# Optimization experiments

Hardware: AMD Instinct MI355X
Metric: run time of the kernel (lower is better)

The kernel has to match this reference:

```python
import jax, jax.numpy as jnp
import numpy as np

B, T, D, H, LAT = 512, 8, 512, 512, 64
NSTEPS = 4  # fixed RK4 steps per observation interval (replaces adaptive dopri5)


def _lin(key, out_dim, in_dim):
    k1, k2 = jax.random.split(key)
    s = 1.0 / np.sqrt(in_dim)
    W = jax.random.uniform(k1, (out_dim, in_dim), minval=-s, maxval=s, dtype=jnp.float32)
    b = jax.random.uniform(k2, (out_dim,), minval=-s, maxval=s, dtype=jnp.float32)
    return W, b


def setup_inputs() -> dict:
    key = jax.random.key(0)
    ks = jax.random.split(key, 8)
    x = jax.random.normal(ks[0], (B, T, D), dtype=jnp.float32)
    # strictly increasing per-sample observation times
    ts = jnp.cumsum(jax.random.uniform(ks[1], (B, T), dtype=jnp.float32) + 0.05, axis=1)
    Wih, bih = _lin(ks[2], 3 * H, D)      # GRU input weights
    Whh, bhh = _lin(ks[3], 3 * H, H)      # GRU hidden weights
    Wout, bout = _lin(ks[4], 2 * LAT, H)  # h2o head: mean/logvar of latent
    W1, b1 = _lin(ks[5], 2 * H, H + 1)    # LatentODEfunc fc1 (state + time)
    W2, b2 = _lin(ks[6], 2 * H, 2 * H)    # fc2
    W3, b3 = _lin(ks[7], H, 2 * H)        # fc3
    return dict(x=x, ts=ts, Wih=Wih, Whh=Whh, bih=bih, bhh=bhh,
                Wout=Wout, bout=bout, W1=W1, b1=b1, W2=W2, b2=b2, W3=W3, b3=b3)


def reference(x, ts, Wih, Whh, bih, bhh, Wout, bout, W1, b1, W2, b2, W3, b3):
    swish = lambda v: v * jax.nn.sigmoid(v)

    def odefunc(t, h):  # t: (B,), h: (B,H) -> dh/dt (B,H)
        z = jnp.concatenate([h, t[:, None]], axis=1)
        z = swish(z @ W1.T + b1)
        z = swish(z @ W2.T + b2)
        return z @ W3.T + b3

    def ode_integrate(h, t0, t1):  # batched RK4 with per-sample dt
        dt = (t1 - t0) / NSTEPS  # (B,)
        def body(carry, _):
            h, t = carry
            d = dt[:, None]
            k1 = odefunc(t, h)
            k2 = odefunc(t + dt / 2, h + d * k1 / 2)
            k3 = odefunc(t + dt / 2, h + d * k2 / 2)
            k4 = odefunc(t + dt, h + d * k3)
            return (h + d / 6 * (k1 + 2 * k2 + 2 * k3 + k4), t + dt), None
        (h, _), _ = jax.lax.scan(body, (h, t0), None, length=NSTEPS)
        return h

    def gru_cell(obs, h):  # torch GRUCell math
        gi = obs @ Wih.T + bih
        gh = h @ Whh.T + bhh
        ir, iz, inn = jnp.split(gi, 3, axis=1)
        hr, hz, hn = jnp.split(gh, 3, axis=1)
        r = jax.nn.sigmoid(ir + hr)
        zg = jax.nn.sigmoid(iz + hz)
        n = jnp.tanh(inn + r * hn)
        return (1.0 - zg) * n + zg * h

    # first interval has zero length -> RK4 with dt=0 leaves h0 unchanged (no ODE at t=0)
    t_prev = jnp.concatenate([ts[:, :1], ts[:, :-1]], axis=1)

    def step(carry, inputs):
        h, c = carry
        obs, t0, t1 = inputs
        h = ode_integrate(h, t0, t1)
        h = gru_cell(obs, h)
        out = h @ Wout.T + bout  # (B, 2*LAT)
        return (h, c), out

    h0 = jnp.zeros((x.shape[0], H), x.dtype)
    c0 = jnp.zeros_like(h0)
    xs = (jnp.swapaxes(x, 0, 1), t_prev.T, ts.T)  # time-major for scan
    (h, c), outs = jax.lax.scan(step, (h0, c0), xs)
    return outs[-1], h, c
```

## Files before the change

kernel.cpp:

```cpp
#include <hip/hip_runtime.h>
#include <hip/hip_bf16.h>
#include <stdint.h>


#define B_ 512
#define T_ 8
#define H_ 512
#define D_ 512

typedef short short8 __attribute__((ext_vector_type(8)));
typedef float f32x4 __attribute__((ext_vector_type(4)));
typedef __hip_bfloat16 bf16;
typedef unsigned long long u64;

__device__ __forceinline__ float sigm(float x){ return 1.f/(1.f+__expf(-x)); }

#define MFMA16(a,b,c) __builtin_amdgcn_mfma_f32_16x16x32_bf16((a),(b),(c),0,0,0)
#define ALD4(p)   __hip_atomic_load((p), __ATOMIC_RELAXED, __HIP_MEMORY_SCOPE_AGENT)
#define AST8(p,v) __hip_atomic_store((u64*)(p),(v),__ATOMIC_RELAXED,__HIP_MEMORY_SCOPE_AGENT)

__device__ __forceinline__ void wait_ge(unsigned* c, unsigned tgt, int* dead){
  if (threadIdx.x == 0){
    if (!*dead){
      int it = 0;
      while (ALD4(c) < tgt){
        __builtin_amdgcn_s_sleep(1);
        if (++it > 50000000){ *dead = 1; break; }
      }
    }
  }
  __syncthreads();
}
__device__ __forceinline__ void publish(unsigned* c){
  __builtin_amdgcn_s_waitcnt(0);
  __syncthreads();
  if (threadIdx.x == 0)
    __hip_atomic_fetch_add(c, 1u, __ATOMIC_RELAXED, __HIP_MEMORY_SCOPE_AGENT);
}

template<int CH, int SH>
__device__ __forceinline__ void stageC16(bf16* lds, int lstr, const bf16* g, int gstr){
  f32x4 tmp[CH];
#pragma unroll
  for (int j = 0; j < CH; ++j){
    int idx = j*256 + threadIdx.x;
    const bf16* p = g + (size_t)(idx >> SH)*gstr + (size_t)(idx & ((1<<SH)-1))*8;
    asm volatile("global_load_dwordx4 %0, %1, off sc0 sc1" : "=v"(tmp[j]) : "v"(p));
  }
  asm volatile("s_waitcnt vmcnt(0)" ::: "memory");
  __builtin_amdgcn_sched_barrier(0);
#pragma unroll
  for (int j = 0; j < CH; ++j){
    int idx = j*256 + threadIdx.x;
    *(f32x4*)&lds[(idx >> SH)*lstr + (idx & ((1<<SH)-1))*8] = tmp[j];
  }
}
template<int CH, int SH>
__device__ __forceinline__ void stageP(bf16* lds, int lstr, const bf16* g, size_t gstr){
#pragma unroll
  for (int j = 0; j < CH; ++j){
    int idx = j*256 + threadIdx.x;
    *(short8*)&lds[(idx >> SH)*lstr + (idx & ((1<<SH)-1))*8] =
        *(const short8*)(g + (size_t)(idx >> SH)*gstr + (size_t)(idx & ((1<<SH)-1))*8);
  }
}

__device__ __forceinline__ u64 pk4(float a0, float a1, float a2, float a3){
  union { bf16 h[4]; u64 q; } u;
  u.h[0] = __float2bfloat16(a0); u.h[1] = __float2bfloat16(a1);
  u.h[2] = __float2bfloat16(a2); u.h[3] = __float2bfloat16(a3);
  return u.q;
}

__global__ __launch_bounds__(256, 1) void persist_k(
    const bf16* __restrict__ W1hb, const bf16* __restrict__ W2b,
    const bf16* __restrict__ Wfb,  const bf16* __restrict__ W3b,
    const bf16* __restrict__ Woutb,const bf16* __restrict__ Wc3,
    const bf16* __restrict__ xbf,
    const float* __restrict__ b1,  const float* __restrict__ b2,
    const float* __restrict__ b3,  const float* __restrict__ bout,
    const float* __restrict__ bcb3,const float* __restrict__ w1t,
    const float* __restrict__ bf3, const float* __restrict__ ts,
    bf16* wbuf, bf16* hbuf, bf16* z1buf, bf16* z2buf, bf16* zbuf,
    unsigned* cnts, float* dout)
{
  extern __shared__ char smem[];
  bf16* slab = (bf16*)smem;
  float* t0s = (float*)(smem + 66048);
  float* dts = (float*)(smem + 66176);
  int* dead  = (int*)(smem + 66304);

  const int tid = threadIdx.x, lane = tid & 63, wv = tid >> 6;
  const int fr = lane & 15, quad = lane >> 4;
  const int nb = blockIdx.x & 15;
  const int mb = blockIdx.x >> 4;
  const int gm0 = mb * 32;
  const int wm = wv & 1;
  const int wn = wv >> 1;

  unsigned* cz1 = cnts + mb*128;
  unsigned* cz2 = cz1 + 32;
  unsigned* ch  = cz1 + 64;
  unsigned* cg  = cz1 + 96;

  if (tid < 32){
    float t0 = ts[(gm0 + tid)*T_];
    t0s[tid] = t0; dts[tid] = 0.f;
  }
  if (tid == 0) *dead = 0;
  __syncthreads();

  const int zc0 = 64*nb + 16*wv + quad*4;
  const int kc0 = 32*nb + 16*wn + quad*4;
  const f32x4 b1v  = *(const f32x4*)&b1[zc0];
  const f32x4 w1tv = *(const f32x4*)&w1t[zc0];
  const f32x4 b2v  = *(const f32x4*)&b2[zc0];
  const f32x4 bf3v = *(const f32x4*)&bf3[zc0];
  const f32x4 b3v  = *(const f32x4*)&b3[kc0];
  f32x4 bcv[4];
#pragma unroll
  for (int g = 0; g < 4; ++g)
    bcv[g] = *(const f32x4*)&bcb3[nb*128 + g*32 + 16*wn + quad*4];
  const f32x4 bov = *(const f32x4*)&bout[16*(nb & 7) + quad*4];

  const bf16* w1p = W1hb  + (size_t)(64*nb + 16*wv + fr)*512  + quad*8;
  const bf16* w2p = W2b   + (size_t)(64*nb + 16*wv + fr)*1024 + quad*8;
  const bf16* wfp = Wfb   + (size_t)(64*nb + 16*wv + fr)*1024 + quad*8;
  const bf16* w3p = W3b   + (size_t)(32*nb + 16*wn + fr)*1024 + quad*8;
  const bf16* wop = Woutb + (size_t)(16*(nb & 7) + fr)*512 + quad*8;
  const bf16* wcp[4];
#pragma unroll
  for (int g = 0; g < 4; ++g)
    wcp[g] = Wc3 + (size_t)(nb*128 + g*32 + 16*wn + fr)*1024 + quad*8;

  short8 w2f[32], wff[32];
#pragma unroll
  for (int k = 0; k < 32; ++k) w2f[k] = *(const short8*)(w2p + k*32);
#pragma unroll
  for (int k = 0; k < 32; ++k) wff[k] = *(const short8*)(wfp + k*32);

  float hw0[4]={0,0,0,0}, hw1[4]={0,0,0,0};
  float pacc0[4]={0,0,0,0}, pacc1[4]={0,0,0,0};
  float zacc0[4]={0,0,0,0}, zacc1[4]={0,0,0,0};
  float hreg[4]={0,0,0,0};
  unsigned tz1 = 16, tz2 = 16, tch = 16, tcg = 16;

  {
    const float t0a = t0s[fr], t0b = t0s[16 + fr];
    float v0[4], v1[4];
#pragma unroll
    for (int j = 0; j < 4; ++j){
      v0[j] = t0a*w1tv[j] + b1v[j];
      v1[j] = t0b*w1tv[j] + b1v[j];
      v0[j] *= sigm(v0[j]); v1[j] *= sigm(v1[j]);
    }
    AST8(z1buf + (size_t)(gm0 + fr)*1024 + zc0,      pk4(v0[0],v0[1],v0[2],v0[3]));
    AST8(z1buf + (size_t)(gm0 + 16 + fr)*1024 + zc0, pk4(v1[0],v1[1],v1[2],v1[3]));
    publish(cz1);
  }

  for (int s = 0; s < T_; ++s){
    for (int sub = 0; sub < 4; ++sub){
      for (int e = 1; e <= 4; ++e){
        wait_ge(cz1, tz1, dead); tz1 += 16;
        stageC16<16,7>(slab, 1032, z1buf + (size_t)gm0*1024, 1024);
        __syncthreads();
        {
          f32x4 a0 = {0,0,0,0}, a1 = {0,0,0,0};
#pragma unroll
          for (int k = 0; k < 32; ++k){
            a0 = MFMA16(w2f[k], *(const short8*)&slab[fr*1032      + k*32 + quad*8], a0);
            a1 = MFMA16(w2f[k], *(const short8*)&slab[(16+fr)*1032 + k*32 + quad*8], a1);
          }
          const float wgt = (e == 2 || e == 3) ? 2.f : 1.f;
          float s0[4], s1[4];
#pragma unroll
          for (int j = 0; j < 4; ++j){
            float v0 = a0[j] + b2v[j], v1 = a1[j] + b2v[j];
            s0[j] = v0*sigm(v0); s1[j] = v1*sigm(v1);
            zacc0[j] += wgt*s0[j]; zacc1[j] += wgt*s1[j];
          }
          if (sub == 3 && e == 4){
            AST8(zbuf + (size_t)(gm0 + fr)*1024 + zc0,      pk4(zacc0[0],zacc0[1],zacc0[2],zacc0[3]));
            AST8(zbuf + (size_t)(gm0 + 16 + fr)*1024 + zc0, pk4(zacc1[0],zacc1[1],zacc1[2],zacc1[3]));
#pragma unroll
            for (int j = 0; j < 4; ++j){ zacc0[j] = 0.f; zacc1[j] = 0.f; }
          } else {
            AST8(z2buf + (size_t)(gm0 + fr)*1024 + zc0,      pk4(s0[0],s0[1],s0[2],s0[3]));
            AST8(z2buf + (size_t)(gm0 + 16 + fr)*1024 + zc0, pk4(s1[0],s1[1],s1[2],s1[3]));
          }
          publish(cz2);
        }
        if (!(sub == 3 && e == 4)){
          wait_ge(cz2, tz2, dead); tz2 += 16;
          stageC16<16,7>(slab, 1032, z2buf + (size_t)gm0*1024, 1024);
          __syncthreads();
          f32x4 p0 = {0,0,0,0}, p1 = {0,0,0,0};
#pragma unroll
          for (int k = 0; k < 32; ++k){
            p0 = MFMA16(wff[k], *(const short8*)&slab[fr*1032      + k*32 + quad*8], p0);
            p1 = MFMA16(wff[k], *(const short8*)&slab[(16+fr)*1032 + k*32 + quad*8], p1);
          }
          const float dta = dts[fr], dtb = dts[16 + fr];
          const float t0a = t0s[fr], t0b = t0s[16 + fr];
          const float ce = (e <= 2) ? (float)sub + 0.5f : (float)sub + 1.f;
          float v0[4], v1[4];
          if (e < 4){
            const float c = (e == 3) ? 1.f : 0.5f;
            const float wgt = (e == 2 || e == 3) ? 2.f : 1.f;
            if (sub < 3){
#pragma unroll
              for (int j = 0; j < 4; ++j){ pacc0[j] += wgt*p0[j]; pacc1[j] += wgt*p1[j]; }
            }
#pragma unroll
            for (int j = 0; j < 4; ++j){
              v0[j] = hw0[j] + c*dta*(p0[j] + bf3v[j]) + (t0a + dta*ce)*w1tv[j] + b1v[j];
              v1[j] = hw1[j] + c*dtb*(p1[j] + bf3v[j]) + (t0b + dtb*ce)*w1tv[j] + b1v[j];
            }
          } else {
#pragma unroll
            for (int j = 0; j < 4; ++j){
              float pa = pacc0[j] + p0[j], pb = pacc1[j] + p1[j];
              hw0[j] += dta*(1.f/6.f)*pa + dta*bf3v[j];
              hw1[j] += dtb*(1.f/6.f)*pb + dtb*bf3v[j];
              pacc0[j] = 0.f; pacc1[j] = 0.f;
              v0[j] = hw0[j] + (t0a + dta*ce)*w1tv[j] + b1v[j];
              v1[j] = hw1[j] + (t0b + dtb*ce)*w1tv[j] + b1v[j];
            }
          }
#pragma unroll
          for (int j = 0; j < 4; ++j){ v0[j] *= sigm(v0[j]); v1[j] *= sigm(v1[j]); }
          AST8(z1buf + (size_t)(gm0 + fr)*1024 + zc0,      pk4(v0[0],v0[1],v0[2],v0[3]));
          AST8(z1buf + (size_t)(gm0 + 16 + fr)*1024 + zc0, pk4(v1[0],v1[1],v1[2],v1[3]));
          publish(cz1);
        }
      }
    }
    wait_ge(cz2, tz2, dead); tz2 += 16;
    stageC16<16,7>(slab, 1032, zbuf + (size_t)gm0*1024, 1024);
    __syncthreads();
    {
      f32x4 ak = {0,0,0,0};
#pragma unroll 8
      for (int k = 0; k < 32; ++k){
        ak = MFMA16(*(const short8*)(w3p + k*32),
                    *(const short8*)&slab[(wm*16 + fr)*1032 + k*32 + quad*8], ak);
      }
      const int r = wm*16 + fr;
      const float dtv = dts[r];
#pragma unroll
      for (int j = 0; j < 4; ++j)
        hreg[j] = hreg[j] + dtv*(1.f/6.f)*ak[j] + 4.f*dtv*b3v[j];
      AST8(hbuf + (size_t)(gm0 + r)*512 + kc0, pk4(hreg[0],hreg[1],hreg[2],hreg[3]));
      publish(ch);
    }
    wait_ge(ch, tch, dead); tch += 16;
    stageC16<8,6>(slab, 1032, hbuf + (size_t)gm0*512, 512);
    stageP<8,6>(slab + 512, 1032, xbf + ((size_t)gm0*T_ + s)*512, (size_t)T_*512);
    __syncthreads();
    {
      f32x4 ag[4] = {{0,0,0,0},{0,0,0,0},{0,0,0,0},{0,0,0,0}};
#pragma unroll 4
      for (int k = 0; k < 32; ++k){
        short8 xv = *(const short8*)&slab[(wm*16 + fr)*1032 + k*32 + quad*8];
#pragma unroll
        for (int g = 0; g < 4; ++g)
          ag[g] = MFMA16(*(const short8*)(wcp[g] + k*32), xv, ag[g]);
      }
      const int r = wm*16 + fr;
#pragma unroll
      for (int j = 0; j < 4; ++j){
        float r_ = sigm(ag[0][j] + bcv[0][j]);
        float z_ = sigm(ag[1][j] + bcv[1][j]);
        float hn = ag[2][j] + bcv[2][j];
        float in = ag[3][j] + bcv[3][j];
        float n_ = tanhf(in + r_*hn);
        hreg[j] = (1.f - z_)*n_ + z_*hreg[j];
      }
      AST8(wbuf + (size_t)(gm0 + r)*512 + kc0, pk4(hreg[0],hreg[1],hreg[2],hreg[3]));
      if (s == T_-1){
        f32x4 hv; hv[0]=hreg[0]; hv[1]=hreg[1]; hv[2]=hreg[2]; hv[3]=hreg[3];
        *(f32x4*)&dout[(size_t)B_*128 + (size_t)(gm0 + r)*512 + kc0] = hv;
        f32x4 z4 = {0,0,0,0};
        *(f32x4*)&dout[(size_t)B_*128 + (size_t)B_*512 + (size_t)(gm0 + r)*512 + kc0] = z4;
      }
      if (tid < 32){
        float t0n = ts[(gm0 + tid)*T_ + s];
        float t1  = (s < T_-1) ? ts[(gm0 + tid)*T_ + s + 1] : t0n;
        t0s[tid] = t0n; dts[tid] = (t1 - t0n)*0.25f;
      }
      publish(cg);
    }
    if (s < T_-1){
      wait_ge(cg, tcg, dead); tcg += 16;
      stageC16<8,6>(slab, 520, wbuf + (size_t)gm0*512, 512);
      __syncthreads();
      f32x4 a0 = {0,0,0,0}, a1 = {0,0,0,0};
#pragma unroll 4
      for (int k = 0; k < 16; ++k){
        short8 wt = *(const short8*)(w1p + k*32);
        a0 = MFMA16(wt, *(const short8*)&slab[fr*520      + k*32 + quad*8], a0);
        a1 = MFMA16(wt, *(const short8*)&slab[(16+fr)*520 + k*32 + quad*8], a1);
      }
      const float t0a = t0s[fr], t0b = t0s[16 + fr];
      float v0[4], v1[4];
#pragma unroll
      for (int j = 0; j < 4; ++j){
        hw0[j] = a0[j]; hw1[j] = a1[j];
        v0[j] = hw0[j] + t0a*w1tv[j] + b1v[j];
        v1[j] = hw1[j] + t0b*w1tv[j] + b1v[j];
        v0[j] *= sigm(v0[j]); v1[j] *= sigm(v1[j]);
      }
      AST8(z1buf + (size_t)(gm0 + fr)*1024 + zc0,      pk4(v0[0],v0[1],v0[2],v0[3]));
      AST8(z1buf + (size_t)(gm0 + 16 + fr)*1024 + zc0, pk4(v1[0],v1[1],v1[2],v1[3]));
      publish(cz1);
    }
  }
  wait_ge(cg, tcg, dead); tcg += 16;
  stageC16<8,6>(slab, 520, wbuf + (size_t)gm0*512, 512);
  __syncthreads();
  if (nb < 8 && wv < 2){
    f32x4 ao = {0,0,0,0};
#pragma unroll 4
    for (int k = 0; k < 16; ++k){
      ao = MFMA16(*(const short8*)(wop + k*32),
                  *(const short8*)&slab[(wv*16 + fr)*520 + k*32 + quad*8], ao);
    }
    f32x4 o;
#pragma unroll
    for (int j = 0; j < 4; ++j) o[j] = ao[j] + bov[j];
    *(f32x4*)&dout[(size_t)(gm0 + wv*16 + fr)*128 + 16*nb + quad*4] = o;
  }
}

__global__ void conv_k(const float* __restrict__ in, bf16* __restrict__ out,
                       int rows, int kin, int kout)
{
  int idx = blockIdx.x*256 + threadIdx.x;
  if (idx >= rows*kout) return;
  int r = idx / kout, k = idx - r*kout;
  out[idx] = __float2bfloat16(k < kin ? in[(size_t)r*kin + k] : 0.f);
}

__global__ void w1t_k(const float* __restrict__ W1, float* __restrict__ w1t)
{
  int i = blockIdx.x*256 + threadIdx.x;
  if (i < 1024) w1t[i] = W1[(size_t)i*513 + 512];
}

__global__ void wf_k(const float* __restrict__ W1, const float* __restrict__ W3,
                     bf16* __restrict__ Wfb)
{
  __shared__ float At[64][64];
  __shared__ float Bt[64][65];
  const int i0 = blockIdx.y*64, j0 = blockIdx.x*64;
  const int tid = threadIdx.x;
  const int ty = tid >> 4, tx = tid & 15;
  float acc[4][4] = {};
  for (int kc = 0; kc < 512; kc += 64){
#pragma unroll
    for (int t = 0; t < 16; ++t){
      int idx = t*256 + tid;
      int r = idx >> 6, k = idx & 63;
      At[r][k] = W1[(size_t)(i0 + r)*513 + kc + k];
      Bt[r][k] = W3[(size_t)(kc + r)*1024 + j0 + k];
    }
    __syncthreads();
#pragma unroll 8
    for (int k = 0; k < 64; ++k){
      float a[4], b[4];
#pragma unroll
      for (int ii = 0; ii < 4; ++ii) a[ii] = At[ty*4 + ii][k];
#pragma unroll
      for (int jj = 0; jj < 4; ++jj) b[jj] = Bt[k][tx*4 + jj];
#pragma unroll
      for (int ii = 0; ii < 4; ++ii)
#pragma unroll
        for (int jj = 0; jj < 4; ++jj) acc[ii][jj] += a[ii]*b[jj];
    }
    __syncthreads();
  }
#pragma unroll
  for (int ii = 0; ii < 4; ++ii)
#pragma unroll
    for (int jj = 0; jj < 4; ++jj)
      Wfb[(size_t)(i0 + ty*4 + ii)*1024 + j0 + tx*4 + jj] = __float2bfloat16(acc[ii][jj]);
}

__global__ void bf3_k(const float* __restrict__ W1, const float* __restrict__ b3,
                      float* __restrict__ bf3)
{
  int i = blockIdx.x*256 + threadIdx.x;
  if (i < 1024){
    float acc = 0.f;
    for (int c = 0; c < 512; ++c) acc += W1[(size_t)i*513 + c]*b3[c];
    bf3[i] = acc;
  }
}

__global__ void wc3_k(const float* __restrict__ Wih, const float* __restrict__ Whh,
                      const float* __restrict__ bih, const float* __restrict__ bhh,
                      bf16* __restrict__ Wc3, float* __restrict__ bcb3)
{
  int idx = blockIdx.x*256 + threadIdx.x;
  if (idx >= 2048*1024) return;
  int R = idx >> 10, k = idx & 1023;
  int n16 = R >> 7, g = (R >> 5) & 3, c = R & 31;
  int hc = n16*32 + c;
  float v;
  if      (g == 0) v = (k < 512) ? Whh[(size_t)hc*512 + k]        : Wih[(size_t)hc*512 + k - 512];
  else if (g == 1) v = (k < 512) ? Whh[(size_t)(512+hc)*512 + k]  : Wih[(size_t)(512+hc)*512 + k - 512];
  else if (g == 2) v = (k < 512) ? Whh[(size_t)(1024+hc)*512 + k] : 0.f;
  else             v = (k < 512) ? 0.f                             : Wih[(size_t)(1024+hc)*512 + k - 512];
  Wc3[idx] = __float2bfloat16(v);
  if (k == 0){
    if      (g == 0) bcb3[R] = bih[hc] + bhh[hc];
    else if (g == 1) bcb3[R] = bih[512 + hc] + bhh[512 + hc];
    else if (g == 2) bcb3[R] = bhh[1024 + hc];
    else             bcb3[R] = bih[1024 + hc];
  }
}

__global__ void init_k(unsigned* __restrict__ cnts)
{
  int idx = blockIdx.x*256 + threadIdx.x;
  if (idx < 16*128) cnts[idx] = 0u;
}

extern "C" void kernel_launch(void* const* d_in, const int* in_sizes, int n_in,
                              void* d_out, int out_size, void* d_ws, size_t ws_size,
                              hipStream_t stream)
{
  const float* x    = (const float*)d_in[0];
  const float* ts   = (const float*)d_in[1];
  const float* Wih  = (const float*)d_in[2];
  const float* Whh  = (const float*)d_in[3];
  const float* bih  = (const float*)d_in[4];
  const float* bhh  = (const float*)d_in[5];
  const float* Wout = (const float*)d_in[6];
  const float* bout = (const float*)d_in[7];
  const float* W1   = (const float*)d_in[8];
  const float* b1   = (const float*)d_in[9];
  const float* W2   = (const float*)d_in[10];
  const float* b2   = (const float*)d_in[11];
  const float* W3   = (const float*)d_in[12];
  const float* b3   = (const float*)d_in[13];

  char* ws = (char*)d_ws;
  size_t off = 0;
  auto alloc = [&](size_t n){ void* p = ws + off; off += (n + 255) & ~(size_t)255; return p; };

  bf16* xbf   = (bf16*)alloc((size_t)B_*T_*D_*2);
  bf16* W1hb  = (bf16*)alloc((size_t)1024*512*2);
  bf16* W2b   = (bf16*)alloc((size_t)1024*1024*2);
  bf16* Wfb   = (bf16*)alloc((size_t)1024*1024*2);
  bf16* W3b   = (bf16*)alloc((size_t)512*1024*2);
  bf16* Woutb = (bf16*)alloc((size_t)128*512*2);
  bf16* Wc3   = (bf16*)alloc((size_t)2048*1024*2);
  float* bcb3 = (float*)alloc((size_t)2048*4);
  float* w1t  = (float*)alloc((size_t)1024*4);
  float* bf3  = (float*)alloc((size_t)1024*4);
  bf16* wbuf  = (bf16*)alloc((size_t)B_*H_*2);
  bf16* hbuf  = (bf16*)alloc((size_t)B_*H_*2);
  bf16* z1buf = (bf16*)alloc((size_t)B_*1024*2);
  bf16* z2buf = (bf16*)alloc((size_t)B_*1024*2);
  bf16* zbuf  = (bf16*)alloc((size_t)B_*1024*2);
  unsigned* cnts = (unsigned*)alloc((size_t)16*128*4);

  auto conv = [&](const float* in, bf16* out, int rows, int kin, int kout){
    int n = rows*kout;
    conv_k<<<(n + 255)/256, 256, 0, stream>>>(in, out, rows, kin, kout);
  };
  conv(x, xbf, B_*T_, D_, D_);
  conv(W1, W1hb, 1024, 513, 512);
  conv(W2, W2b, 1024, 1024, 1024);
  conv(W3, W3b, 512, 1024, 1024);
  conv(Wout, Woutb, 128, 512, 512);
  w1t_k<<<4, 256, 0, stream>>>(W1, w1t);
  wf_k<<<dim3(16,16), 256, 0, stream>>>(W1, W3, Wfb);
  bf3_k<<<4, 256, 0, stream>>>(W1, b3, bf3);
  wc3_k<<<(2048*1024)/256, 256, 0, stream>>>(Wih, Whh, bih, bhh, Wc3, bcb3);
  init_k<<<8, 256, 0, stream>>>(cnts);

  (void)hipFuncSetAttribute((const void*)persist_k,
                            hipFuncAttributeMaxDynamicSharedMemorySize, 66560);
  persist_k<<<256, 256, 66560, stream>>>(
      W1hb, W2b, Wfb, W3b, Woutb, Wc3, xbf,
      b1, b2, b3, bout, bcb3, w1t, bf3, ts,
      wbuf, hbuf, z1buf, z2buf, zbuf, cnts, (float*)d_out);
}
```

Before: 1.822 ms.

## Co-locate row-group blocks on one XCD and use L2-coherent exchange when confirmed

Changes the block-to-tile mapping so the 16 blocks sharing a row group (mb) get block IDs that are congruent mod 8, which under round-robin dispatch should place them on the same XCD. Each block reads its XCC_ID from a hardware register and checks through a global table that all its peers report the same one. If they do, the inter-block exchange buffers are written and read with sc0 only (L2 scope) instead of sc0 sc1 system-coherent accesses, cutting the latency of the per-stage handoffs. This adds a startup handshake, and it depends on the dispatch-placement assumption; when the check fails it falls back to the old coherent path.

Result: faster. 1.565 ms (-14.1%).

```diff
diff --git a/kernel.cpp b/kernel.cpp
--- a/kernel.cpp
+++ b/kernel.cpp
@@ -17,7 +17,6 @@
 
 #define MFMA16(a,b,c) __builtin_amdgcn_mfma_f32_16x16x32_bf16((a),(b),(c),0,0,0)
 #define ALD4(p)   __hip_atomic_load((p), __ATOMIC_RELAXED, __HIP_MEMORY_SCOPE_AGENT)
-#define AST8(p,v) __hip_atomic_store((u64*)(p),(v),__ATOMIC_RELAXED,__HIP_MEMORY_SCOPE_AGENT)
 
 __device__ __forceinline__ void wait_ge(unsigned* c, unsigned tgt, int* dead){
   if (threadIdx.x == 0){
@@ -38,14 +37,21 @@
     __hip_atomic_fetch_add(c, 1u, __ATOMIC_RELAXED, __HIP_MEMORY_SCOPE_AGENT);
 }
 
-template<int CH, int SH>
+template<bool L2C>
+__device__ __forceinline__ void ast8c(void* p, u64 v){
+  if (L2C) asm volatile("global_store_dwordx2 %0, %1, off sc0" :: "v"(p), "v"(v) : "memory");
+  else     __hip_atomic_store((u64*)p, v, __ATOMIC_RELAXED, __HIP_MEMORY_SCOPE_AGENT);
+}
+
+template<int CH, int SH, bool L2C>
 __device__ __forceinline__ void stageC16(bf16* lds, int lstr, const bf16* g, int gstr){
   f32x4 tmp[CH];
 #pragma unroll
   for (int j = 0; j < CH; ++j){
     int idx = j*256 + threadIdx.x;
     const bf16* p = g + (size_t)(idx >> SH)*gstr + (size_t)(idx & ((1<<SH)-1))*8;
-    asm volatile("global_load_dwordx4 %0, %1, off sc0 sc1" : "=v"(tmp[j]) : "v"(p));
+    if (L2C) asm volatile("global_load_dwordx4 %0, %1, off sc0"     : "=v"(tmp[j]) : "v"(p));
+    else     asm volatile("global_load_dwordx4 %0, %1, off sc0 sc1" : "=v"(tmp[j]) : "v"(p));
   }
   asm volatile("s_waitcnt vmcnt(0)" ::: "memory");
   __builtin_amdgcn_sched_barrier(0);
@@ -71,6 +77,8 @@
   u.h[2] = __float2bfloat16(a2); u.h[3] = __float2bfloat16(a3);
   return u.q;
 }
+
+template<bool V> struct BC { static constexpr bool value = V; };
 
 __global__ __launch_bounds__(256, 1) void persist_k(
     const bf16* __restrict__ W1hb, const bf16* __restrict__ W2b,
@@ -82,18 +90,20 @@
     const float* __restrict__ bcb3,const float* __restrict__ w1t,
     const float* __restrict__ bf3, const float* __restrict__ ts,
     bf16* wbuf, bf16* hbuf, bf16* z1buf, bf16* z2buf, bf16* zbuf,
-    unsigned* cnts, float* dout)
+    unsigned* cnts, unsigned* xtab, float* dout)
 {
   extern __shared__ char smem[];
   bf16* slab = (bf16*)smem;
   float* t0s = (float*)(smem + 66048);
   float* dts = (float*)(smem + 66176);
   int* dead  = (int*)(smem + 66304);
+  int* fflag = (int*)(smem + 66308);
 
   const int tid = threadIdx.x, lane = tid & 63, wv = tid >> 6;
   const int fr = lane & 15, quad = lane >> 4;
-  const int nb = blockIdx.x & 15;
-  const int mb = blockIdx.x >> 4;
+  const int bId = blockIdx.x;
+  const int mb = (bId & 7) + 8*(bId >> 7);
+  const int nb = (bId >> 3) & 15;
   const int gm0 = mb * 32;
   const int wm = wv & 1;
   const int wn = wv >> 1;
@@ -103,12 +113,38 @@
   unsigned* ch  = cz1 + 64;
   unsigned* cg  = cz1 + 96;
 
+  unsigned myxcd;
+  asm volatile("s_getreg_b32 %0, hwreg(HW_REG_XCC_ID)" : "=s"(myxcd));
+  myxcd = (myxcd & 0x7fffffffu) | 0x80000000u;
+  if (tid == 0)
+    __hip_atomic_store(&xtab[bId], myxcd, __ATOMIC_RELAXED, __HIP_MEMORY_SCOPE_AGENT);
+
   if (tid < 32){
     float t0 = ts[(gm0 + tid)*T_];
     t0s[tid] = t0; dts[tid] = 0.f;
   }
   if (tid == 0) *dead = 0;
+
+  if (tid == 0){
+    unsigned ref = 0; int ok = 1;
+    for (int j = 0; j < 16; ++j){
+      int bj = (mb & 7) + 8*j + 128*(mb >> 3);
+      unsigned v; int it = 0;
+      do {
+        v = ALD4(&xtab[bj]);
+        if (!v){
+          __builtin_amdgcn_s_sleep(8);
+          if (++it > 200000){ ok = 0; break; }
+        }
+      } while (!v);
+      if (!v){ ok = 0; break; }
+      if (j == 0) ref = v;
+      else if (v != ref){ ok = 0; break; }
+    }
+    *fflag = ok && (ref != 0);
+  }
   __syncthreads();
+  const int fastp = *fflag;
 
   const int zc0 = 64*nb + 16*wv + quad*4;
   const int kc0 = 32*nb + 16*wn + quad*4;
@@ -145,180 +181,186 @@
   float hreg[4]={0,0,0,0};
   unsigned tz1 = 16, tz2 = 16, tch = 16, tcg = 16;
 
-  {
-    const float t0a = t0s[fr], t0b = t0s[16 + fr];
-    float v0[4], v1[4];
-#pragma unroll
-    for (int j = 0; j < 4; ++j){
-      v0[j] = t0a*w1tv[j] + b1v[j];
-      v1[j] = t0b*w1tv[j] + b1v[j];
-      v0[j] *= sigm(v0[j]); v1[j] *= sigm(v1[j]);
-    }
-    AST8(z1buf + (size_t)(gm0 + fr)*1024 + zc0,      pk4(v0[0],v0[1],v0[2],v0[3]));
-    AST8(z1buf + (size_t)(gm0 + 16 + fr)*1024 + zc0, pk4(v1[0],v1[1],v1[2],v1[3]));
-    publish(cz1);
-  }
-
-  for (int s = 0; s < T_; ++s){
-    for (int sub = 0; sub < 4; ++sub){
-      for (int e = 1; e <= 4; ++e){
-        wait_ge(cz1, tz1, dead); tz1 += 16;
-        stageC16<16,7>(slab, 1032, z1buf + (size_t)gm0*1024, 1024);
-        __syncthreads();
-        {
-          f32x4 a0 = {0,0,0,0}, a1 = {0,0,0,0};
-#pragma unroll
-          for (int k = 0; k < 32; ++k){
-            a0 = MFMA16(w2f[k], *(const short8*)&slab[fr*1032      + k*32 + quad*8], a0);
-            a1 = MFMA16(w2f[k], *(const short8*)&slab[(16+fr)*1032 + k*32 + quad*8], a1);
-          }
-          const float wgt = (e == 2 || e == 3) ? 2.f : 1.f;
-          float s0[4], s1[4];
-#pragma unroll
-          for (int j = 0; j < 4; ++j){
-            float v0 = a0[j] + b2v[j], v1 = a1[j] + b2v[j];
-            s0[j] = v0*sigm(v0); s1[j] = v1*sigm(v1);
-            zacc0[j] += wgt*s0[j]; zacc1[j] += wgt*s1[j];
-          }
-          if (sub == 3 && e == 4){
-            AST8(zbuf + (size_t)(gm0 + fr)*1024 + zc0,      pk4(zacc0[0],zacc0[1],zacc0[2],zacc0[3]));
-            AST8(zbuf + (size_t)(gm0 + 16 + fr)*1024 + zc0, pk4(zacc1[0],zacc1[1],zacc1[2],zacc1[3]));
-#pragma unroll
-            for (int j = 0; j < 4; ++j){ zacc0[j] = 0.f; zacc1[j] = 0.f; }
-          } else {
-            AST8(z2buf + (size_t)(gm0 + fr)*1024 + zc0,      pk4(s0[0],s0[1],s0[2],s0[3]));
-            AST8(z2buf + (size_t)(gm0 + 16 + fr)*1024 + zc0, pk4(s1[0],s1[1],s1[2],s1[3]));
-          }
-          publish(cz2);
-        }
-        if (!(sub == 3 && e == 4)){
-          wait_ge(cz2, tz2, dead); tz2 += 16;
-          stageC16<16,7>(slab, 1032, z2buf + (size_t)gm0*1024, 1024);
-          __syncthreads();
-          f32x4 p0 = {0,0,0,0}, p1 = {0,0,0,0};
-#pragma unroll
-          for (int k = 0; k < 32; ++k){
-            p0 = MFMA16(wff[k], *(const short8*)&slab[fr*1032      + k*32 + quad*8], p0);
-            p1 = MFMA16(wff[k], *(const short8*)&slab[(16+fr)*1032 + k*32 + quad*8], p1);
-          }
-          const float dta = dts[fr], dtb = dts[16 + fr];
-          const float t0a = t0s[fr], t0b = t0s[16 + fr];
-          const float ce = (e <= 2) ? (float)sub + 0.5f : (float)sub + 1.f;
-          float v0[4], v1[4];
-          if (e < 4){
-            const float c = (e == 3) ? 1.f : 0.5f;
-            const float wgt = (e == 2 || e == 3) ? 2.f : 1.f;
-            if (sub < 3){
-#pragma unroll
-              for (int j = 0; j < 4; ++j){ pacc0[j] += wgt*p0[j]; pacc1[j] += wgt*p1[j]; }
-            }
-#pragma unroll
-            for (int j = 0; j < 4; ++j){
-              v0[j] = hw0[j] + c*dta*(p0[j] + bf3v[j]) + (t0a + dta*ce)*w1tv[j] + b1v[j];
-              v1[j] = hw1[j] + c*dtb*(p1[j] + bf3v[j]) + (t0b + dtb*ce)*w1tv[j] + b1v[j];
-            }
-          } else {
-#pragma unroll
-            for (int j = 0; j < 4; ++j){
-              float pa = pacc0[j] + p0[j], pb = pacc1[j] + p1[j];
-              hw0[j] += dta*(1.f/6.f)*pa + dta*bf3v[j];
-              hw1[j] += dtb*(1.f/6.f)*pb + dtb*bf3v[j];
-              pacc0[j] = 0.f; pacc1[j] = 0.f;
-              v0[j] = hw0[j] + (t0a + dta*ce)*w1tv[j] + b1v[j];
-              v1[j] = hw1[j] + (t0b + dtb*ce)*w1tv[j] + b1v[j];
-            }
-          }
-#pragma unroll
-          for (int j = 0; j < 4; ++j){ v0[j] *= sigm(v0[j]); v1[j] *= sigm(v1[j]); }
-          AST8(z1buf + (size_t)(gm0 + fr)*1024 + zc0,      pk4(v0[0],v0[1],v0[2],v0[3]));
-          AST8(z1buf + (size_t)(gm0 + 16 + fr)*1024 + zc0, pk4(v1[0],v1[1],v1[2],v1[3]));
-          publish(cz1);
-        }
-      }
-    }
-    wait_ge(cz2, tz2, dead); tz2 += 16;
-    stageC16<16,7>(slab, 1032, zbuf + (size_t)gm0*1024, 1024);
-    __syncthreads();
+  auto body = [&](auto FASTC){
+    constexpr bool FC = decltype(FASTC)::value;
+
     {
-      f32x4 ak = {0,0,0,0};
-#pragma unroll 8
-      for (int k = 0; k < 32; ++k){
-        ak = MFMA16(*(const short8*)(w3p + k*32),
-                    *(const short8*)&slab[(wm*16 + fr)*1032 + k*32 + quad*8], ak);
-      }
-      const int r = wm*16 + fr;
-      const float dtv = dts[r];
-#pragma unroll
-      for (int j = 0; j < 4; ++j)
-        hreg[j] = hreg[j] + dtv*(1.f/6.f)*ak[j] + 4.f*dtv*b3v[j];
-      AST8(hbuf + (size_t)(gm0 + r)*512 + kc0, pk4(hreg[0],hreg[1],hreg[2],hreg[3]));
-      publish(ch);
-    }
-    wait_ge(ch, tch, dead); tch += 16;
-    stageC16<8,6>(slab, 1032, hbuf + (size_t)gm0*512, 512);
-    stageP<8,6>(slab + 512, 1032, xbf + ((size_t)gm0*T_ + s)*512, (size_t)T_*512);
-    __syncthreads();
-    {
-      f32x4 ag[4] = {{0,0,0,0},{0,0,0,0},{0,0,0,0},{0,0,0,0}};
-#pragma unroll 4
-      for (int k = 0; k < 32; ++k){
-        short8 xv = *(const short8*)&slab[(wm*16 + fr)*1032 + k*32 + quad*8];
-#pragma unroll
-        for (int g = 0; g < 4; ++g)
-          ag[g] = MFMA16(*(const short8*)(wcp[g] + k*32), xv, ag[g]);
-      }
-      const int r = wm*16 + fr;
-#pragma unroll
-      for (int j = 0; j < 4; ++j){
-        float r_ = sigm(ag[0][j] + bcv[0][j]);
-        float z_ = sigm(ag[1][j] + bcv[1][j]);
-        float hn = ag[2][j] + bcv[2][j];
-        float in = ag[3][j] + bcv[3][j];
-        float n_ = tanhf(in + r_*hn);
-        hreg[j] = (1.f - z_)*n_ + z_*hreg[j];
-      }
-      AST8(wbuf + (size_t)(gm0 + r)*512 + kc0, pk4(hreg[0],hreg[1],hreg[2],hreg[3]));
-      if (s == T_-1){
-        f32x4 hv; hv[0]=hreg[0]; hv[1]=hreg[1]; hv[2]=hreg[2]; hv[3]=hreg[3];
-        *(f32x4*)&dout[(size_t)B_*128 + (size_t)(gm0 + r)*512 + kc0] = hv;
-        f32x4 z4 = {0,0,0,0};
-        *(f32x4*)&dout[(size_t)B_*128 + (size_t)B_*512 + (size_t)(gm0 + r)*512 + kc0] = z4;
-      }
-      if (tid < 32){
-        float t0n = ts[(gm0 + tid)*T_ + s];
-        float t1  = (s < T_-1) ? ts[(gm0 + tid)*T_ + s + 1] : t0n;
-        t0s[tid] = t0n; dts[tid] = (t1 - t0n)*0.25f;
-      }
-      publish(cg);
-    }
-    if (s < T_-1){
-      wait_ge(cg, tcg, dead); tcg += 16;
-      stageC16<8,6>(slab, 520, wbuf + (size_t)gm0*512, 512);
-      __syncthreads();
-      f32x4 a0 = {0,0,0,0}, a1 = {0,0,0,0};
-#pragma unroll 4
-      for (int k = 0; k < 16; ++k){
-        short8 wt = *(const short8*)(w1p + k*32);
-        a0 = MFMA16(wt, *(const short8*)&slab[fr*520      + k*32 + quad*8], a0);
-        a1 = MFMA16(wt, *(const short8*)&slab[(16+fr)*520 + k*32 + quad*8], a1);
-      }
       const float t0a = t0s[fr], t0b = t0s[16 + fr];
       float v0[4], v1[4];
 #pragma unroll
       for (int j = 0; j < 4; ++j){
-        hw0[j] = a0[j]; hw1[j] = a1[j];
-        v0[j] = hw0[j] + t0a*w1tv[j] + b1v[j];
-        v1[j] = hw1[j] + t0b*w1tv[j] + b1v[j];
+        v0[j] = t0a*w1tv[j] + b1v[j];
+        v1[j] = t0b*w1tv[j] + b1v[j];
         v0[j] *= sigm(v0[j]); v1[j] *= sigm(v1[j]);
       }
-      AST8(z1buf + (size_t)(gm0 + fr)*1024 + zc0,      pk4(v0[0],v0[1],v0[2],v0[3]));
-      AST8(z1buf + (size_t)(gm0 + 16 + fr)*1024 + zc0, pk4(v1[0],v1[1],v1[2],v1[3]));
+      ast8c<FC>(z1buf + (size_t)(gm0 + fr)*1024 + zc0,      pk4(v0[0],v0[1],v0[2],v0[3]));
+      ast8c<FC>(z1buf + (size_t)(gm0 + 16 + fr)*1024 + zc0, pk4(v1[0],v1[1],v1[2],v1[3]));
       publish(cz1);
     }
-  }
-  wait_ge(cg, tcg, dead); tcg += 16;
-  stageC16<8,6>(slab, 520, wbuf + (size_t)gm0*512, 512);
-  __syncthreads();
+
+    for (int s = 0; s < T_; ++s){
+      for (int sub = 0; sub < 4; ++sub){
+        for (int e = 1; e <= 4; ++e){
+          wait_ge(cz1, tz1, dead); tz1 += 16;
+          stageC16<16,7,FC>(slab, 1032, z1buf + (size_t)gm0*1024, 1024);
+          __syncthreads();
+          {
+            f32x4 a0 = {0,0,0,0}, a1 = {0,0,0,0};
+#pragma unroll
+            for (int k = 0; k < 32; ++k){
+              a0 = MFMA16(w2f[k], *(const short8*)&slab[fr*1032      + k*32 + quad*8], a0);
+              a1 = MFMA16(w2f[k], *(const short8*)&slab[(16+fr)*1032 + k*32 + quad*8], a1);
+            }
+            const float wgt = (e == 2 || e == 3) ? 2.f : 1.f;
+            float s0[4], s1[4];
+#pragma unroll
+            for (int j = 0; j < 4; ++j){
+              float v0 = a0[j] + b2v[j], v1 = a1[j] + b2v[j];
+              s0[j] = v0*sigm(v0); s1[j] = v1*sigm(v1);
+              zacc0[j] += wgt*s0[j]; zacc1[j] += wgt*s1[j];
+            }
+            if (sub == 3 && e == 4){
+              ast8c<FC>(zbuf + (size_t)(gm0 + fr)*1024 + zc0,      pk4(zacc0[0],zacc0[1],zacc0[2],zacc0[3]));
+              ast8c<FC>(zbuf + (size_t)(gm0 + 16 + fr)*1024 + zc0, pk4(zacc1[0],zacc1[1],zacc1[2],zacc1[3]));
+#pragma unroll
+              for (int j = 0; j < 4; ++j){ zacc0[j] = 0.f; zacc1[j] = 0.f; }
+            } else {
+              ast8c<FC>(z2buf + (size_t)(gm0 + fr)*1024 + zc0,      pk4(s0[0],s0[1],s0[2],s0[3]));
+              ast8c<FC>(z2buf + (size_t)(gm0 + 16 + fr)*1024 + zc0, pk4(s1[0],s1[1],s1[2],s1[3]));
+            }
+            publish(cz2);
+          }
+          if (!(sub == 3 && e == 4)){
+            wait_ge(cz2, tz2, dead); tz2 += 16;
+            stageC16<16,7,FC>(slab, 1032, z2buf + (size_t)gm0*1024, 1024);
+            __syncthreads();
+            f32x4 p0 = {0,0,0,0}, p1 = {0,0,0,0};
+#pragma unroll
+            for (int k = 0; k < 32; ++k){
+              p0 = MFMA16(wff[k], *(const short8*)&slab[fr*1032      + k*32 + quad*8], p0);
+              p1 = MFMA16(wff[k], *(const short8*)&slab[(16+fr)*1032 + k*32 + quad*8], p1);
+            }
+            const float dta = dts[fr], dtb = dts[16 + fr];
+            const float t0a = t0s[fr], t0b = t0s[16 + fr];
+            const float ce = (e <= 2) ? (float)sub + 0.5f : (float)sub + 1.f;
+            float v0[4], v1[4];
+            if (e < 4){
+              const float c = (e == 3) ? 1.f : 0.5f;
+              const float wgt = (e == 2 || e == 3) ? 2.f : 1.f;
+              if (sub < 3){
+#pragma unroll
+                for (int j = 0; j < 4; ++j){ pacc0[j] += wgt*p0[j]; pacc1[j] += wgt*p1[j]; }
+              }
+#pragma unroll
+              for (int j = 0; j < 4; ++j){
+                v0[j] = hw0[j] + c*dta*(p0[j] + bf3v[j]) + (t0a + dta*ce)*w1tv[j] + b1v[j];
+                v1[j] = hw1[j] + c*dtb*(p1[j] + bf3v[j]) + (t0b + dtb*ce)*w1tv[j] + b1v[j];
+              }
+            } else {
+#pragma unroll
+              for (int j = 0; j < 4; ++j){
+                float pa = pacc0[j] + p0[j], pb = pacc1[j] + p1[j];
+                hw0[j] += dta*(1.f/6.f)*pa + dta*bf3v[j];
+                hw1[j] += dtb*(1.f/6.f)*pb + dtb*bf3v[j];
+                pacc0[j] = 0.f; pacc1[j] = 0.f;
+                v0[j] = hw0[j] + (t0a + dta*ce)*w1tv[j] + b1v[j];
+                v1[j] = hw1[j] + (t0b + dtb*ce)*w1tv[j] + b1v[j];
+              }
+            }
+#pragma unroll
+            for (int j = 0; j < 4; ++j){ v0[j] *= sigm(v0[j]); v1[j] *= sigm(v1[j]); }
+            ast8c<FC>(z1buf + (size_t)(gm0 + fr)*1024 + zc0,      pk4(v0[0],v0[1],v0[2],v0[3]));
+            ast8c<FC>(z1buf + (size_t)(gm0 + 16 + fr)*1024 + zc0, pk4(v1[0],v1[1],v1[2],v1[3]));
+            publish(cz1);
+          }
+        }
+      }
+      wait_ge(cz2, tz2, dead); tz2 += 16;
+      stageC16<16,7,FC>(slab, 1032, zbuf + (size_t)gm0*1024, 1024);
+      __syncthreads();
+      {
+        f32x4 ak = {0,0,0,0};
+#pragma unroll 8
+        for (int k = 0; k < 32; ++k){
+          ak = MFMA16(*(const short8*)(w3p + k*32),
+                      *(const short8*)&slab[(wm*16 + fr)*1032 + k*32 + quad*8], ak);
+        }
+        const int r = wm*16 + fr;
+        const float dtv = dts[r];
+#pragma unroll
+        for (int j = 0; j < 4; ++j)
+          hreg[j] = hreg[j] + dtv*(1.f/6.f)*ak[j] + 4.f*dtv*b3v[j];
+        ast8c<FC>(hbuf + (size_t)(gm0 + r)*512 + kc0, pk4(hreg[0],hreg[1],hreg[2],hreg[3]));
+        publish(ch);
+      }
+      wait_ge(ch, tch, dead); tch += 16;
+      stageC16<8,6,FC>(slab, 1032, hbuf + (size_t)gm0*512, 512);
+      stageP<8,6>(slab + 512, 1032, xbf + ((size_t)gm0*T_ + s)*512, (size_t)T_*512);
+      __syncthreads();
+      {
+        f32x4 ag[4] = {{0,0,0,0},{0,0,0,0},{0,0,0,0},{0,0,0,0}};
+#pragma unroll 4
+        for (int k = 0; k < 32; ++k){
+          short8 xv = *(const short8*)&slab[(wm*16 + fr)*1032 + k*32 + quad*8];
+#pragma unroll
+          for (int g = 0; g < 4; ++g)
+            ag[g] = MFMA16(*(const short8*)(wcp[g] + k*32), xv, ag[g]);
+        }
+        const int r = wm*16 + fr;
+#pragma unroll
+        for (int j = 0; j < 4; ++j){
+          float r_ = sigm(ag[0][j] + bcv[0][j]);
+          float z_ = sigm(ag[1][j] + bcv[1][j]);
+          float hn = ag[2][j] + bcv[2][j];
+          float in = ag[3][j] + bcv[3][j];
+          float n_ = tanhf(in + r_*hn);
+          hreg[j] = (1.f - z_)*n_ + z_*hreg[j];
+        }
+        ast8c<FC>(wbuf + (size_t)(gm0 + r)*512 + kc0, pk4(hreg[0],hreg[1],hreg[2],hreg[3]));
+        if (s == T_-1){
+          f32x4 hv; hv[0]=hreg[0]; hv[1]=hreg[1]; hv[2]=hreg[2]; hv[3]=hreg[3];
+          *(f32x4*)&dout[(size_t)B_*128 + (size_t)(gm0 + r)*512 + kc0] = hv;
+          f32x4 z4 = {0,0,0,0};
+          *(f32x4*)&dout[(size_t)B_*128 + (size_t)B_*512 + (size_t)(gm0 + r)*512 + kc0] = z4;
+        }
+        if (tid < 32){
+          float t0n = ts[(gm0 + tid)*T_ + s];
+          float t1  = (s < T_-1) ? ts[(gm0 + tid)*T_ + s + 1] : t0n;
+          t0s[tid] = t0n; dts[tid] = (t1 - t0n)*0.25f;
+        }
+        publish(cg);
+      }
+      if (s < T_-1){
+        wait_ge(cg, tcg, dead); tcg += 16;
+        stageC16<8,6,FC>(slab, 520, wbuf + (size_t)gm0*512, 512);
+        __syncthreads();
+        f32x4 a0 = {0,0,0,0}, a1 = {0,0,0,0};
+#pragma unroll 4
+        for (int k = 0; k < 16; ++k){
+          short8 wt = *(const short8*)(w1p + k*32);
+          a0 = MFMA16(wt, *(const short8*)&slab[fr*520      + k*32 + quad*8], a0);
+          a1 = MFMA16(wt, *(const short8*)&slab[(16+fr)*520 + k*32 + quad*8], a1);
+        }
+        const float t0a = t0s[fr], t0b = t0s[16 + fr];
+        float v0[4], v1[4];
+#pragma unroll
+        for (int j = 0; j < 4; ++j){
+          hw0[j] = a0[j]; hw1[j] = a1[j];
+          v0[j] = hw0[j] + t0a*w1tv[j] + b1v[j];
+          v1[j] = hw1[j] + t0b*w1tv[j] + b1v[j];
+          v0[j] *= sigm(v0[j]); v1[j] *= sigm(v1[j]);
+        }
+        ast8c<FC>(z1buf + (size_t)(gm0 + fr)*1024 + zc0,      pk4(v0[0],v0[1],v0[2],v0[3]));
+        ast8c<FC>(z1buf + (size_t)(gm0 + 16 + fr)*1024 + zc0, pk4(v1[0],v1[1],v1[2],v1[3]));
+        publish(cz1);
+      }
+    }
+    wait_ge(cg, tcg, dead); tcg += 16;
+    stageC16<8,6,FC>(slab, 520, wbuf + (size_t)gm0*512, 512);
+    __syncthreads();
+  };
+  if (fastp) body(BC<true>{}); else body(BC<false>{});
+
   if (nb < 8 && wv < 2){
     f32x4 ao = {0,0,0,0};
 #pragma unroll 4
@@ -421,10 +463,11 @@
   }
 }
 
-__global__ void init_k(unsigned* __restrict__ cnts)
+__global__ void init_k(unsigned* __restrict__ cnts, unsigned* __restrict__ xtab)
 {
   int idx = blockIdx.x*256 + threadIdx.x;
   if (idx < 16*128) cnts[idx] = 0u;
+  if (idx < 256) xtab[idx] = 0u;
 }
 
 extern "C" void kernel_launch(void* const* d_in, const int* in_sizes, int n_in,
@@ -466,6 +509,7 @@
   bf16* z2buf = (bf16*)alloc((size_t)B_*1024*2);
   bf16* zbuf  = (bf16*)alloc((size_t)B_*1024*2);
   unsigned* cnts = (unsigned*)alloc((size_t)16*128*4);
+  unsigned* xtab = (unsigned*)alloc((size_t)256*4);
 
   auto conv = [&](const float* in, bf16* out, int rows, int kin, int kout){
     int n = rows*kout;
@@ -480,12 +524,12 @@
   wf_k<<<dim3(16,16), 256, 0, stream>>>(W1, W3, Wfb);
   bf3_k<<<4, 256, 0, stream>>>(W1, b3, bf3);
   wc3_k<<<(2048*1024)/256, 256, 0, stream>>>(Wih, Whh, bih, bhh, Wc3, bcb3);
-  init_k<<<8, 256, 0, stream>>>(cnts);
+  init_k<<<8, 256, 0, stream>>>(cnts, xtab);
 
   (void)hipFuncSetAttribute((const void*)persist_k,
                             hipFuncAttributeMaxDynamicSharedMemorySize, 66560);
   persist_k<<<256, 256, 66560, stream>>>(
       W1hb, W2b, Wfb, W3b, Woutb, Wc3, xbf,
       b1, b2, b3, bout, bcb3, w1t, bf3, ts,
-      wbuf, hbuf, z1buf, z2buf, zbuf, cnts, (float*)d_out);
-}
+      wbuf, hbuf, z1buf, z2buf, zbuf, cnts, xtab, (float*)d_out);
+}
```
